# Kernel optimization log

Measured on AMD Instinct MI355X. Metric: run time of the kernel, lower is better.

## Reference

```python
import jax, jax.numpy as jnp
import numpy as np

B = 65536
DIM = 256       # latent_dim
N_EMBED = 1024  # codebook size


def setup_inputs() -> dict:
    key = jax.random.key(0)
    kx, ke = jax.random.split(key)
    x = jax.random.normal(kx, (B, DIM), dtype=jnp.float32)
    # rosinality Quantize stores codebook as embed[dim, n_embed]
    embed = jax.random.normal(ke, (DIM, N_EMBED), dtype=jnp.float32)
    return {"x": x, "embed": embed}


def reference(x, embed):
    # dist[b, k] = ||x_b||^2 - 2 x_b . e_k + ||e_k||^2  (negated for argmax in
    # the original; equivalent to argmin of the distance)
    x_sq = jnp.sum(x * x, axis=1, keepdims=True)            # [B, 1]
    e_sq = jnp.sum(embed * embed, axis=0, keepdims=True)    # [1, K]
    dist = x_sq - 2.0 * (x @ embed) + e_sq                  # [B, K]
    embed_ind = jnp.argmin(dist, axis=1)                    # [B] int
    # codebook lookup: embed.T is [K, dim]
    quantize = jnp.take(embed.T, embed_ind, axis=0)         # [B, dim]
    # commitment loss term
    diff = jnp.mean(jnp.square(jax.lax.stop_gradient(quantize) - x))
    # straight-through estimator
    quantize_st = x + jax.lax.stop_gradient(quantize - x)
    return quantize_st, diff, embed_ind
```

## Files before the change

kernel.cpp:

```cpp
#include <hip/hip_runtime.h>

#define NROWSQ   65536
#define NDIM     256
#define NCB      1024
#define DIFF_OFF 16777216
#define IDX_OFF  16777217

#define MARGIN_A 0.35f
#define MARGIN_B 1.5e-3f
#define SCORE_SHIFT 384.0f

typedef __attribute__((ext_vector_type(8))) short s16x8;
typedef __attribute__((ext_vector_type(4))) float f32x4;

__device__ __forceinline__ unsigned short f2bf(float f) {
  union { float f; unsigned u; } v; v.f = f;
  return (unsigned short)((v.u + 0x7FFFu + ((v.u >> 16) & 1u)) >> 16);
}

__device__ __forceinline__ void top2_update(float& v1, int& i1, float& v2, int& i2,
                                            float v, int col) {
  if (v > v1 || (v == v1 && col < i1)) { v2 = v1; i2 = i1; v1 = v; i1 = col; }
  else if (v > v2 || (v == v2 && col < i2)) { v2 = v; i2 = col; }
}
__device__ __forceinline__ void top2_merge(float& v1, int& i1, float& v2, int& i2,
                                           float ov1, int oi1, float ov2, int oi2) {
  if (ov1 > v1 || (ov1 == v1 && oi1 < i1)) {
    float nv2 = v1; int ni2 = i1;
    if (ov2 > nv2 || (ov2 == nv2 && oi2 < ni2)) { nv2 = ov2; ni2 = oi2; }
    v1 = ov1; i1 = oi1; v2 = nv2; i2 = ni2;
  } else if (ov1 > v2 || (ov1 == v2 && oi1 < i2)) {
    v2 = ov1; i2 = oi1;
  }
}

__device__ __forceinline__ float np_pairwise128(const float* p) {
  float r0 = p[0], r1 = p[1], r2 = p[2], r3 = p[3];
  float r4 = p[4], r5 = p[5], r6 = p[6], r7 = p[7];
  for (int i = 8; i < 128; i += 8) {
    r0 += p[i];     r1 += p[i + 1]; r2 += p[i + 2]; r3 += p[i + 3];
    r4 += p[i + 4]; r5 += p[i + 5]; r6 += p[i + 6]; r7 += p[i + 7];
  }
  return ((r0 + r1) + (r2 + r3)) + ((r4 + r5) + (r6 + r7));
}

__global__ void k0a_transpose(const float* __restrict__ E, float* __restrict__ embT,
                              unsigned short* __restrict__ cbT,
                              int* __restrict__ cntA, int* __restrict__ cntB) {
  __shared__ float T[64][65];
  const int t = threadIdx.x;
  const int kbase = (blockIdx.x & 15) * 64;
  const int dbase = (blockIdx.x >> 4) * 64;
  if (blockIdx.x == 0 && t == 0) { *cntA = 0; *cntB = 0; }
  #pragma unroll
  for (int i = 0; i < 4; ++i) {
    const int cid = i * 256 + t;
    const int dl = cid >> 4, kc = cid & 15;
    const float4 v = *(const float4*)(E + (size_t)(dbase + dl) * NCB + kbase + kc * 4);
    T[dl][kc * 4 + 0] = v.x; T[dl][kc * 4 + 1] = v.y;
    T[dl][kc * 4 + 2] = v.z; T[dl][kc * 4 + 3] = v.w;
  }
  __syncthreads();
  #pragma unroll
  for (int i = 0; i < 4; ++i) {
    const int cid = i * 256 + t;
    const int kl = cid >> 4, dc = cid & 15;
    float4 v;
    v.x = T[dc * 4 + 0][kl]; v.y = T[dc * 4 + 1][kl];
    v.z = T[dc * 4 + 2][kl]; v.w = T[dc * 4 + 3][kl];
    *(float4*)(embT + (size_t)(kbase + kl) * NDIM + dbase + dc * 4) = v;
    ushort4 b;
    b.x = f2bf(v.x); b.y = f2bf(v.y); b.z = f2bf(v.z); b.w = f2bf(v.w);
    *(ushort4*)(cbT + (size_t)(kbase + kl) * NDIM + dbase + dc * 4) = b;
  }
}

__global__ void k0b_esq(const float* __restrict__ embT, float* __restrict__ esq32,
                        float* __restrict__ esqs, float* __restrict__ esqr) {
  const int b = blockIdx.x, t = threadIdx.x;
  if (b < 128) {
    const int col = b * 8 + (t >> 5);
    const int l = t & 31;
    double s = 0.0;
    #pragma unroll
    for (int i = 0; i < 8; ++i) {
      const double v = (double)embT[(size_t)col * NDIM + l + i * 32];
      s += v * v;
    }
    #pragma unroll
    for (int m = 16; m >= 1; m >>= 1) s += __shfl_xor(s, m);
    if (l == 0) {
      esq32[col] = (float)(0.5 * s);
      esqs[col] = (float)(0.5 * s) - SCORE_SHIFT;
    }
  } else {
    const int col = (b - 128) * 256 + t;
    float sr = 0.f;
    for (int d = 0; d < NDIM; ++d) {
      const float v = embT[(size_t)col * NDIM + d];
      sr = sr + v * v;
    }
    esqr[col] = sr;
  }
}

#define BLD 264

__global__ void k1_scores(
    const float* __restrict__ X, const unsigned short* __restrict__ cbT,
    const float* __restrict__ esqs, int2* __restrict__ part1) {
  __shared__ __align__(16) unsigned short Bs[64 * BLD];
  __shared__ float esq_l[512];
  const int t = threadIdx.x;
  const int lane = t & 63, w = t >> 6;
  const int l15 = lane & 15, quad = lane >> 4;
  const int half = blockIdx.x & 1;
  const int rowbase = (blockIdx.x >> 1) * 128;
  const int colbase = half * 512;

  {
    const float2 e2 = *(const float2*)(esqs + colbase + t * 2);
    *(float2*)(esq_l + t * 2) = e2;
  }

  s16x8 afrag[2][8];
  #pragma unroll
  for (int m = 0; m < 2; ++m) {
    const float* xr = X + (size_t)(rowbase + w * 32 + m * 16 + l15) * NDIM;
    #pragma unroll
    for (int ks = 0; ks < 8; ++ks) {
      const float4 xa = *(const float4*)(xr + ks * 32 + quad * 8);
      const float4 xb = *(const float4*)(xr + ks * 32 + quad * 8 + 4);
      s16x8 a;
      a[0] = (short)f2bf(xa.x); a[1] = (short)f2bf(xa.y);
      a[2] = (short)f2bf(xa.z); a[3] = (short)f2bf(xa.w);
      a[4] = (short)f2bf(xb.x); a[5] = (short)f2bf(xb.y);
      a[6] = (short)f2bf(xb.z); a[7] = (short)f2bf(xb.w);
      afrag[m][ks] = a;
    }
  }

  int key1[2][4], key2[2][4];
  #pragma unroll
  for (int m = 0; m < 2; ++m)
    #pragma unroll
    for (int r = 0; r < 4; ++r) { key1[m][r] = 0; key2[m][r] = 0; }

  for (int nt = 0; nt < 8; ++nt) {
    __syncthreads();
    #pragma unroll
    for (int i = 0; i < 8; ++i) {
      const int id = i * 256 + t;
      const int c = id >> 5, d8 = id & 31;
      *(uint4*)&Bs[c * BLD + d8 * 8] =
          *(const uint4*)(cbT + (size_t)(colbase + nt * 64 + c) * NDIM + d8 * 8);
    }
    __syncthreads();

    f32x4 acc[2][4];
    #pragma unroll
    for (int m = 0; m < 2; ++m)
      #pragma unroll
      for (int s = 0; s < 4; ++s) acc[m][s] = (f32x4){0.f, 0.f, 0.f, 0.f};

    #pragma unroll
    for (int ks = 0; ks < 8; ++ks) {
      #pragma unroll
      for (int s = 0; s < 4; ++s) {
        const s16x8 b = *(const s16x8*)&Bs[(s * 16 + l15) * BLD + ks * 32 + quad * 8];
        acc[0][s] = __builtin_amdgcn_mfma_f32_16x16x32_bf16(afrag[0][ks], b, acc[0][s], 0, 0, 0);
        acc[1][s] = __builtin_amdgcn_mfma_f32_16x16x32_bf16(afrag[1][ks], b, acc[1][s], 0, 0, 0);
      }
    }

    #pragma unroll
    for (int s = 0; s < 4; ++s) {
      const int lcol = nt * 64 + s * 16 + l15;
      const float eq = esq_l[lcol];
      const int suffix = 1023 - (colbase + lcol);
      #pragma unroll
      for (int m = 0; m < 2; ++m)
        #pragma unroll
        for (int r = 0; r < 4; ++r) {
          float sc = acc[m][s][r] - eq;
          sc = fmaxf(sc, 1.0f);
          const int key = (__float_as_int(sc) & 0xFFFFFC00) | suffix;
          key2[m][r] = max(key2[m][r], min(key1[m][r], key));
          key1[m][r] = max(key1[m][r], key);
        }
    }
  }

  #pragma unroll
  for (int mask = 1; mask <= 8; mask <<= 1) {
    #pragma unroll
    for (int m = 0; m < 2; ++m)
      #pragma unroll
      for (int r = 0; r < 4; ++r) {
        const int ok1 = __shfl_xor(key1[m][r], mask);
        const int ok2 = __shfl_xor(key2[m][r], mask);
        const int n1 = max(key1[m][r], ok1);
        const int n2 = max(min(key1[m][r], ok1), max(key2[m][r], ok2));
        key1[m][r] = n1; key2[m][r] = n2;
      }
  }

  if (l15 == 0) {
    #pragma unroll
    for (int m = 0; m < 2; ++m)
      #pragma unroll
      for (int r = 0; r < 4; ++r) {
        const int grow = rowbase + w * 32 + m * 16 + quad * 4 + r;
        part1[half * NROWSQ + grow] = make_int2(key1[m][r], key2[m][r]);
      }
  }
}

__global__ void k1m_merge(const int2* __restrict__ part1, float* __restrict__ outIdx,
                          int* __restrict__ cntA, int* __restrict__ listA,
                          float* __restrict__ outDiff) {
  const int row = blockIdx.x * 256 + threadIdx.x;
  if (row == 0) *outDiff = 0.f;
  const int2 a = part1[row];
  const int2 b = part1[NROWSQ + row];
  const int k1 = max(a.x, b.x);
  const int k2 = max(min(a.x, b.x), max(a.y, b.y));
  outIdx[row] = (float)(1023 - (k1 & 1023));
  const float g1 = __int_as_float(k1 & 0xFFFFFC00);
  const float g2 = __int_as_float(k2 & 0xFFFFFC00);
  if (g1 - g2 < MARGIN_A) {
    const int p = atomicAdd(cntA, 1);
    listA[p] = row;
  }
}

__global__ __launch_bounds__(256) void k2a_refine(
    const float* __restrict__ X, const float* __restrict__ E,
    const float* __restrict__ esq, const int* __restrict__ cntA,
    const int* __restrict__ listA, float4* __restrict__ part2) {
  __shared__ float Xs[8][NDIM];
  __shared__ float rv1[4][8], rv2[4][8];
  __shared__ int   ri1[4][8], ri2[4][8];
  const int t = threadIdx.x;
  const int lane = t & 63, w = t >> 6;
  const int half = blockIdx.x & 1;
  const int bstride = gridDim.x >> 1;
  const int cnt = *cntA;
  const int k0 = half * 512 + t * 2;
  for (int base = (blockIdx.x >> 1) * 8; base < cnt; base += bstride * 8) {
    const int nrows = min(8, cnt - base);
    __syncthreads();
    for (int r = 0; r < 8; ++r) {
      const int rid = listA[base + min(r, nrows - 1)];
      Xs[r][t] = X[(size_t)rid * NDIM + t];
    }
    __syncthreads();

    float acc[8][2];
    #pragma unroll
    for (int r = 0; r < 8; ++r) { acc[r][0] = 0.f; acc[r][1] = 0.f; }

    for (int d = 0; d < NDIM; ++d) {
      const float2 e = *(const float2*)(E + d * NCB + k0);
      #pragma unroll
      for (int r = 0; r < 8; ++r) {
        const float x = Xs[r][d];
        acc[r][0] += x * e.x; acc[r][1] += x * e.y;
      }
    }
    const float eq0 = esq[k0], eq1 = esq[k0 + 1];

    #pragma unroll
    for (int r = 0; r < 8; ++r) {
      float bv1 = -3.4e38f, bv2 = -3.4e38f; int bi1 = 0x7fffffff, bi2 = 0x7fffffff;
      top2_update(bv1, bi1, bv2, bi2, acc[r][0] - eq0, k0);
      top2_update(bv1, bi1, bv2, bi2, acc[r][1] - eq1, k0 + 1);
      #pragma unroll
      for (int mask = 1; mask < 64; mask <<= 1) {
        const float ov1 = __shfl_xor(bv1, mask); const int oi1 = __shfl_xor(bi1, mask);
        const float ov2 = __shfl_xor(bv2, mask); const int oi2 = __shfl_xor(bi2, mask);
        top2_merge(bv1, bi1, bv2, bi2, ov1, oi1, ov2, oi2);
      }
      if (lane == 0) { rv1[w][r] = bv1; ri1[w][r] = bi1; rv2[w][r] = bv2; ri2[w][r] = bi2; }
    }
    __syncthreads();
    if (t < nrows) {
      const int r = t;
      float fv1 = rv1[0][r], fv2 = rv2[0][r]; int fi1 = ri1[0][r], fi2 = ri2[0][r];
      for (int ww = 1; ww < 4; ++ww)
        top2_merge(fv1, fi1, fv2, fi2, rv1[ww][r], ri1[ww][r], rv2[ww][r], ri2[ww][r]);
      part2[half * NROWSQ + base + r] = make_float4(fv1, (float)fi1, fv2, (float)fi2);
    }
    __syncthreads();
  }
}

__global__ void k2m_merge(const float4* __restrict__ part2, const int* __restrict__ cntA,
                          const int* __restrict__ listA, float* __restrict__ outIdx,
                          int* __restrict__ cntB, int* __restrict__ listB) {
  const int cnt = *cntA;
  for (int j = blockIdx.x * 256 + threadIdx.x; j < cnt; j += gridDim.x * 256) {
    const float4 a = part2[j];
    const float4 b = part2[NROWSQ + j];
    float v1 = a.x, v2 = a.z; int i1 = (int)a.y, i2 = (int)a.w;
    top2_merge(v1, i1, v2, i2, b.x, (int)b.y, b.z, (int)b.w);
    const int rid = listA[j];
    outIdx[rid] = (float)i1;
    if (v1 - v2 < MARGIN_B) { const int p = atomicAdd(cntB, 1); listB[p] = rid; }
  }
}

__global__ __launch_bounds__(256) void k2b_mimic(
    const float* __restrict__ X, const float* __restrict__ embT,
    const float* __restrict__ esqr, const int* __restrict__ cntB,
    const int* __restrict__ listB, float* __restrict__ outIdx) {
  __shared__ float Xr[NDIM];
  __shared__ float Psq[NDIM];
  __shared__ float rv[256];
  __shared__ int ri[256];
  const int t = threadIdx.x;
  const int cnt = *cntB;
  for (int j = blockIdx.x; j < cnt; j += gridDim.x) {
    const int rid = listB[j];
    __syncthreads();
    {
      const float x = X[(size_t)rid * NDIM + t];
      Xr[t] = x;
      Psq[t] = x * x;
    }
    __syncthreads();
    const float x_sq = np_pairwise128(Psq) + np_pairwise128(Psq + 128);

    float best = 3.4e38f; int bidx = 0x7fffffff;
    #pragma unroll
    for (int c = 0; c < 4; ++c) {
      const int k = t + c * 256;
      const float* er = embT + (size_t)k * NDIM;
      float acc = 0.f;
      #pragma unroll 8
      for (int dq = 0; dq < 64; ++dq) {
        const float4 e = *(const float4*)(er + dq * 4);
        const float4 x = *(const float4*)(Xr + dq * 4);
        acc = fmaf(x.x, e.x, acc);
        acc = fmaf(x.y, e.y, acc);
        acc = fmaf(x.z, e.z, acc);
        acc = fmaf(x.w, e.w, acc);
      }
      const float dist = (x_sq - 2.0f * acc) + esqr[k];
      if (dist < best || (dist == best && k < bidx)) { best = dist; bidx = k; }
    }
    rv[t] = best; ri[t] = bidx;
    __syncthreads();
    for (int off = 128; off > 0; off >>= 1) {
      if (t < off) {
        if (rv[t + off] < rv[t] || (rv[t + off] == rv[t] && ri[t + off] < ri[t])) {
          rv[t] = rv[t + off]; ri[t] = ri[t + off];
        }
      }
      __syncthreads();
    }
    if (t == 0) outIdx[rid] = (float)ri[0];
  }
}

__global__ __launch_bounds__(256) void k4_outputs(
    const float* __restrict__ X, const float* __restrict__ embT,
    const float* __restrict__ idxF, float* __restrict__ outQ,
    float* __restrict__ outDiff) {
  const int t = threadIdx.x;
  const int lane = t & 63, w = t >> 6;
  const int W = blockIdx.x * 4 + w;
  float s = 0.f;
  #pragma unroll
  for (int i = 0; i < 8; ++i) {
    const int r = W + i * 8192;
    const int idx = (int)idxF[r];
    const float4 q = *(const float4*)(embT + idx * NDIM + lane * 4);
    const float4 x = *(const float4*)(X + (size_t)r * NDIM + lane * 4);
    *(float4*)(outQ + (size_t)r * NDIM + lane * 4) = q;
    const float dx = q.x - x.x, dy = q.y - x.y, dz = q.z - x.z, dw = q.w - x.w;
    s += dx * dx + dy * dy + dz * dz + dw * dw;
  }
  #pragma unroll
  for (int mask = 1; mask < 64; mask <<= 1) s += __shfl_xor(s, mask);
  __shared__ float bs[4];
  if (lane == 0) bs[w] = s;
  __syncthreads();
  if (t == 0)
    atomicAdd(outDiff, (bs[0] + bs[1] + bs[2] + bs[3]) * (1.0f / 16777216.0f));
}

extern "C" void kernel_launch(void* const* d_in, const int* in_sizes, int n_in,
                              void* d_out, int out_size, void* d_ws, size_t ws_size,
                              hipStream_t stream) {
  const float* X = (const float*)d_in[0];
  const float* E = (const float*)d_in[1];
  float* out = (float*)d_out;

  char* ws = (char*)d_ws;
  unsigned short* cbT = (unsigned short*)(ws + 0x000000);
  float*  embT  = (float*) (ws + 0x080000);
  float*  esq32 = (float*) (ws + 0x180000);
  float*  esqs  = (float*) (ws + 0x181000);
  float*  esqr  = (float*) (ws + 0x182000);
  int* cntA  = (int*)(ws + 0x183000);
  int* cntB  = (int*)(ws + 0x183004);
  int* listA = (int*)(ws + 0x183100);
  int* listB = (int*)(ws + 0x1C3100);
  int2*   part1 = (int2*)  (ws + 0x203100);
  float4* part2 = (float4*)(ws + 0x303100);

  float* outQ    = out;
  float* outDiff = out + DIFF_OFF;
  float* outIdx  = out + IDX_OFF;

  k0a_transpose<<<dim3(64), dim3(256), 0, stream>>>(E, embT, cbT, cntA, cntB);
  k0b_esq<<<dim3(132), dim3(256), 0, stream>>>(embT, esq32, esqs, esqr);
  k1_scores<<<dim3(1024), dim3(256), 0, stream>>>(X, cbT, esqs, part1);
  k1m_merge<<<dim3(256), dim3(256), 0, stream>>>(part1, outIdx, cntA, listA, outDiff);
  k2a_refine<<<dim3(1024), dim3(256), 0, stream>>>(X, E, esq32, cntA, listA, part2);
  k2m_merge<<<dim3(64), dim3(256), 0, stream>>>(part2, cntA, listA, outIdx, cntB, listB);
  k2b_mimic<<<dim3(64), dim3(256), 0, stream>>>(X, embT, esqr, cntB, listB, outIdx);
  k4_outputs<<<dim3(2048), dim3(256), 0, stream>>>(X, embT, outIdx, outQ, outDiff);
}
```

Before: 344.6 us.

## Fuse codebook prep kernels, prefetch B tiles in registers, swizzle LDS, fold bias into accumulator

Merges the transpose and norm kernels into a single prep kernel that computes the norms directly from the original codebook layout, saving one launch. In the scoring kernel, the next codebook tile is prefetched into registers while the current tile is consumed. The padded LDS layout is replaced by an XOR-swizzled one to avoid bank conflicts. The accumulators are initialised with the shifted negative norm, which removes the per-element subtract and clamp. Dropping the clamp to 1.0 assumes scores stay positive; if they do not, the integer-key ordering could break. The fused norm loop reads the codebook with strided column accesses.

```diff
diff --git a/kernel.cpp b/kernel.cpp
--- a/kernel.cpp
+++ b/kernel.cpp
@@ -44,72 +44,57 @@
   return ((r0 + r1) + (r2 + r3)) + ((r4 + r5) + (r6 + r7));
 }
 
-__global__ void k0a_transpose(const float* __restrict__ E, float* __restrict__ embT,
-                              unsigned short* __restrict__ cbT,
-                              int* __restrict__ cntA, int* __restrict__ cntB) {
-  __shared__ float T[64][65];
+__global__ void k0_prep(const float* __restrict__ E, float* __restrict__ embT,
+                        unsigned short* __restrict__ cbT, float* __restrict__ esq32,
+                        float* __restrict__ nesq, float* __restrict__ esqr,
+                        int* __restrict__ cntA, int* __restrict__ cntB) {
   const int t = threadIdx.x;
-  const int kbase = (blockIdx.x & 15) * 64;
-  const int dbase = (blockIdx.x >> 4) * 64;
-  if (blockIdx.x == 0 && t == 0) { *cntA = 0; *cntB = 0; }
-  #pragma unroll
-  for (int i = 0; i < 4; ++i) {
-    const int cid = i * 256 + t;
-    const int dl = cid >> 4, kc = cid & 15;
-    const float4 v = *(const float4*)(E + (size_t)(dbase + dl) * NCB + kbase + kc * 4);
-    T[dl][kc * 4 + 0] = v.x; T[dl][kc * 4 + 1] = v.y;
-    T[dl][kc * 4 + 2] = v.z; T[dl][kc * 4 + 3] = v.w;
-  }
-  __syncthreads();
-  #pragma unroll
-  for (int i = 0; i < 4; ++i) {
-    const int cid = i * 256 + t;
-    const int kl = cid >> 4, dc = cid & 15;
-    float4 v;
-    v.x = T[dc * 4 + 0][kl]; v.y = T[dc * 4 + 1][kl];
-    v.z = T[dc * 4 + 2][kl]; v.w = T[dc * 4 + 3][kl];
-    *(float4*)(embT + (size_t)(kbase + kl) * NDIM + dbase + dc * 4) = v;
-    ushort4 b;
-    b.x = f2bf(v.x); b.y = f2bf(v.y); b.z = f2bf(v.z); b.w = f2bf(v.w);
-    *(ushort4*)(cbT + (size_t)(kbase + kl) * NDIM + dbase + dc * 4) = b;
-  }
-}
-
-__global__ void k0b_esq(const float* __restrict__ embT, float* __restrict__ esq32,
-                        float* __restrict__ esqs, float* __restrict__ esqr) {
-  const int b = blockIdx.x, t = threadIdx.x;
-  if (b < 128) {
-    const int col = b * 8 + (t >> 5);
-    const int l = t & 31;
+  if (blockIdx.x < 64) {
+    __shared__ float T[64][65];
+    const int kbase = (blockIdx.x & 15) * 64;
+    const int dbase = (blockIdx.x >> 4) * 64;
+    #pragma unroll
+    for (int i = 0; i < 4; ++i) {
+      const int cid = i * 256 + t;
+      const int dl = cid >> 4, kc = cid & 15;
+      const float4 v = *(const float4*)(E + (size_t)(dbase + dl) * NCB + kbase + kc * 4);
+      T[dl][kc * 4 + 0] = v.x; T[dl][kc * 4 + 1] = v.y;
+      T[dl][kc * 4 + 2] = v.z; T[dl][kc * 4 + 3] = v.w;
+    }
+    __syncthreads();
+    #pragma unroll
+    for (int i = 0; i < 4; ++i) {
+      const int cid = i * 256 + t;
+      const int kl = cid >> 4, dc = cid & 15;
+      float4 v;
+      v.x = T[dc * 4 + 0][kl]; v.y = T[dc * 4 + 1][kl];
+      v.z = T[dc * 4 + 2][kl]; v.w = T[dc * 4 + 3][kl];
+      *(float4*)(embT + (size_t)(kbase + kl) * NDIM + dbase + dc * 4) = v;
+      ushort4 b;
+      b.x = f2bf(v.x); b.y = f2bf(v.y); b.z = f2bf(v.z); b.w = f2bf(v.w);
+      *(ushort4*)(cbT + (size_t)(kbase + kl) * NDIM + dbase + dc * 4) = b;
+    }
+  } else {
+    const int k = (blockIdx.x - 64) * 256 + t;
+    if (blockIdx.x == 64 && t == 0) { *cntA = 0; *cntB = 0; }
     double s = 0.0;
-    #pragma unroll
-    for (int i = 0; i < 8; ++i) {
-      const double v = (double)embT[(size_t)col * NDIM + l + i * 32];
-      s += v * v;
-    }
-    #pragma unroll
-    for (int m = 16; m >= 1; m >>= 1) s += __shfl_xor(s, m);
-    if (l == 0) {
-      esq32[col] = (float)(0.5 * s);
-      esqs[col] = (float)(0.5 * s) - SCORE_SHIFT;
-    }
-  } else {
-    const int col = (b - 128) * 256 + t;
     float sr = 0.f;
     for (int d = 0; d < NDIM; ++d) {
-      const float v = embT[(size_t)col * NDIM + d];
-      sr = sr + v * v;
-    }
-    esqr[col] = sr;
-  }
-}
-
-#define BLD 264
+      const float v = E[d * NCB + k];
+      s += (double)v * (double)v;
+      const float p = v * v;
+      sr = sr + p;
+    }
+    esq32[k] = (float)(0.5 * s);
+    nesq[k] = SCORE_SHIFT - (float)(0.5 * s);
+    esqr[k] = sr;
+  }
+}
 
 __global__ void k1_scores(
     const float* __restrict__ X, const unsigned short* __restrict__ cbT,
-    const float* __restrict__ esqs, int2* __restrict__ part1) {
-  __shared__ __align__(16) unsigned short Bs[64 * BLD];
+    const float* __restrict__ nesq, int2* __restrict__ part1) {
+  __shared__ uint4 Bs[2048];
   __shared__ float esq_l[512];
   const int t = threadIdx.x;
   const int lane = t & 63, w = t >> 6;
@@ -119,9 +104,13 @@
   const int colbase = half * 512;
 
   {
-    const float2 e2 = *(const float2*)(esqs + colbase + t * 2);
+    const float2 e2 = *(const float2*)(nesq + colbase + t * 2);
     *(float2*)(esq_l + t * 2) = e2;
   }
+
+  const int trow = t >> 5;
+  const int tks = (t >> 2) & 7, tquad = t & 3;
+  const uint4* cb4 = (const uint4*)cbT;
 
   s16x8 afrag[2][8];
   #pragma unroll
@@ -146,28 +135,40 @@
     #pragma unroll
     for (int r = 0; r < 4; ++r) { key1[m][r] = 0; key2[m][r] = 0; }
 
+  uint4 p[8];
+  #pragma unroll
+  for (int i = 0; i < 8; ++i)
+    p[i] = cb4[(size_t)(colbase + i * 8 + trow) * 32 + (t & 31)];
+
   for (int nt = 0; nt < 8; ++nt) {
     __syncthreads();
     #pragma unroll
     for (int i = 0; i < 8; ++i) {
-      const int id = i * 256 + t;
-      const int c = id >> 5, d8 = id & 31;
-      *(uint4*)&Bs[c * BLD + d8 * 8] =
-          *(const uint4*)(cbT + (size_t)(colbase + nt * 64 + c) * NDIM + d8 * 8);
-    }
-    __syncthreads();
+      const int c = i * 8 + trow;
+      const int a16 = ((c >> 4) * 8 + tks) * 64 + tquad * 16 + ((c & 15) ^ tks);
+      Bs[a16] = p[i];
+    }
+    __syncthreads();
+    if (nt < 7) {
+      #pragma unroll
+      for (int i = 0; i < 8; ++i)
+        p[i] = cb4[(size_t)(colbase + (nt + 1) * 64 + i * 8 + trow) * 32 + (t & 31)];
+    }
 
     f32x4 acc[2][4];
     #pragma unroll
-    for (int m = 0; m < 2; ++m)
-      #pragma unroll
-      for (int s = 0; s < 4; ++s) acc[m][s] = (f32x4){0.f, 0.f, 0.f, 0.f};
+    for (int s = 0; s < 4; ++s) {
+      const float e = esq_l[nt * 64 + s * 16 + l15];
+      acc[0][s] = (f32x4){e, e, e, e};
+      acc[1][s] = (f32x4){e, e, e, e};
+    }
 
     #pragma unroll
     for (int ks = 0; ks < 8; ++ks) {
       #pragma unroll
       for (int s = 0; s < 4; ++s) {
-        const s16x8 b = *(const s16x8*)&Bs[(s * 16 + l15) * BLD + ks * 32 + quad * 8];
+        const s16x8 b = *(const s16x8*)((const char*)Bs +
+            ((s * 8 + ks) * 1024 + quad * 256 + ((l15 ^ ks) * 16)));
         acc[0][s] = __builtin_amdgcn_mfma_f32_16x16x32_bf16(afrag[0][ks], b, acc[0][s], 0, 0, 0);
         acc[1][s] = __builtin_amdgcn_mfma_f32_16x16x32_bf16(afrag[1][ks], b, acc[1][s], 0, 0, 0);
       }
@@ -175,16 +176,12 @@
 
     #pragma unroll
     for (int s = 0; s < 4; ++s) {
-      const int lcol = nt * 64 + s * 16 + l15;
-      const float eq = esq_l[lcol];
-      const int suffix = 1023 - (colbase + lcol);
+      const int suffix = 1023 - (colbase + nt * 64 + s * 16 + l15);
       #pragma unroll
       for (int m = 0; m < 2; ++m)
         #pragma unroll
         for (int r = 0; r < 4; ++r) {
-          float sc = acc[m][s][r] - eq;
-          sc = fmaxf(sc, 1.0f);
-          const int key = (__float_as_int(sc) & 0xFFFFFC00) | suffix;
+          const int key = (__float_as_int(acc[m][s][r]) & 0xFFFFFC00) | suffix;
           key2[m][r] = max(key2[m][r], min(key1[m][r], key));
           key1[m][r] = max(key1[m][r], key);
         }
@@ -401,7 +398,7 @@
   unsigned short* cbT = (unsigned short*)(ws + 0x000000);
   float*  embT  = (float*) (ws + 0x080000);
   float*  esq32 = (float*) (ws + 0x180000);
-  float*  esqs  = (float*) (ws + 0x181000);
+  float*  nesq  = (float*) (ws + 0x181000);
   float*  esqr  = (float*) (ws + 0x182000);
   int* cntA  = (int*)(ws + 0x183000);
   int* cntB  = (int*)(ws + 0x183004);
@@ -414,9 +411,8 @@
   float* outDiff = out + DIFF_OFF;
   float* outIdx  = out + IDX_OFF;
 
-  k0a_transpose<<<dim3(64), dim3(256), 0, stream>>>(E, embT, cbT, cntA, cntB);
-  k0b_esq<<<dim3(132), dim3(256), 0, stream>>>(embT, esq32, esqs, esqr);
-  k1_scores<<<dim3(1024), dim3(256), 0, stream>>>(X, cbT, esqs, part1);
+  k0_prep<<<dim3(68), dim3(256), 0, stream>>>(E, embT, cbT, esq32, nesq, esqr, cntA, cntB);
+  k1_scores<<<dim3(1024), dim3(256), 0, stream>>>(X, cbT, nesq, part1);
   k1m_merge<<<dim3(256), dim3(256), 0, stream>>>(part1, outIdx, cntA, listA, outDiff);
   k2a_refine<<<dim3(1024), dim3(256), 0, stream>>>(X, E, esq32, cntA, listA, part2);
   k2m_merge<<<dim3(64), dim3(256), 0, stream>>>(part2, cntA, listA, outIdx, cntB, listB);
```

Result: slower. 408.5 us (+18.5%).
